# Kernel tuning notes

Measured on AMD Instinct MI355X. Metric: run time of the kernel, lower is better.

The kernel has to match this reference:

```python
import jax, jax.numpy as jnp
import numpy as np

B, Q, KV, D, H = 2, 2048, 2048, 1024, 16
DH = D // H  # 64


def _rmsnorm(x, w, eps):
    return x * jax.lax.rsqrt(jnp.mean(x * x, axis=-1, keepdims=True) + eps) * w


def setup_inputs() -> dict:
    k0 = jax.random.key(0)
    ks = jax.random.split(k0, 7)
    s = 0.02
    return {
        "query": jax.random.normal(ks[0], (B, Q, D), jnp.float32),
        "key": jax.random.normal(ks[1], (B, KV, D), jnp.float32),
        "value": jax.random.normal(ks[2], (B, KV, D), jnp.float32),
        # RMSNorm weights (init to ones like nn.RMSNorm)
        "wq_norm": jnp.ones((D,), jnp.float32),
        "wk_norm": jnp.ones((D,), jnp.float32),
        # MHA in-projection for q and k (Wv / out_proj never affect attn weights)
        "Wq": jax.random.normal(ks[3], (D, D), jnp.float32) * s,
        "Wk": jax.random.normal(ks[4], (D, D), jnp.float32) * s,
        "bq": jax.random.normal(ks[5], (D,), jnp.float32) * s,
        "bk": jax.random.normal(ks[6], (D,), jnp.float32) * s,
    }


def reference(query, key, value, wq_norm, wk_norm, Wq, Wk, bq, bk):
    eps = jnp.finfo(query.dtype).eps  # nn.RMSNorm default eps
    qn = _rmsnorm(query, wq_norm, eps)
    kn = _rmsnorm(key, wk_norm, eps)
    # MHA in-projections (torch Linear: x @ W.T + b), split into heads
    q = (qn @ Wq.T + bq).reshape(B, Q, H, DH)
    k = (kn @ Wk.T + bk).reshape(B, KV, H, DH)
    # per-head scaled dot-product scores [B,H,Q,KV]
    scores = jnp.einsum('bihd,bjhd->bhij', q, k) / np.float32(np.sqrt(DH))
    # softmax over keys, then average over heads (average_attn_weights=True)
    attn = jax.nn.softmax(scores, axis=-1).mean(axis=1)  # [B,Q,KV]
    # custom re-weighting of the *separate* value tensor
    features = jnp.einsum('bij,bjd->bid', attn, value)  # [B,Q,D]
    return features
```

## Files before the change

kernel.cpp:

```cpp
#include <hip/hip_runtime.h>

#define B_  2
#define Q_  2048
#define KV_ 2048
#define D_  1024
#define H_  16
#define DH_ 64

#define QSCALE 0.18033688011112042f

using u16 = unsigned short;
using bf16x8 = __attribute__((ext_vector_type(8))) short;
using f32x4  = __attribute__((ext_vector_type(4))) float;

__device__ __forceinline__ u16 f2bf(float x) {
  unsigned u = __float_as_uint(x);
  u += 0x7fffu + ((u >> 16) & 1u);
  return (u16)(u >> 16);
}

__device__ __forceinline__ void gl_lds16(const void* g, void* l) {
  __builtin_amdgcn_global_load_lds(
      (const __attribute__((address_space(1))) void*)g,
      (__attribute__((address_space(3))) void*)l, 16, 0, 0);
}

__device__ __forceinline__ int swz_off(int row, int unit) {
  return row * 64 + ((unit ^ (row & 7)) << 3);
}

#define MFMA16(a, b, c) __builtin_amdgcn_mfma_f32_16x16x32_bf16((a), (b), (c), 0, 0, 0)
#define EXP2F(x) __builtin_amdgcn_exp2f(x)

__global__ __launch_bounds__(256) void k_rmsnorm_cast(
    const float* __restrict__ q, const float* __restrict__ k,
    const float* __restrict__ wq, const float* __restrict__ wk,
    u16* __restrict__ qn, u16* __restrict__ kn)
{
  const int row = blockIdx.x;
  const float* src; const float* w; u16* dst;
  if (row < B_ * Q_) {
    src = q + (size_t)row * D_; w = wq; dst = qn + (size_t)row * D_;
  } else {
    const int r2 = row - B_ * Q_;
    src = k + (size_t)r2 * D_; w = wk; dst = kn + (size_t)r2 * D_;
  }
  const int t = threadIdx.x;
  float4 v = reinterpret_cast<const float4*>(src)[t];
  float ss = v.x * v.x + v.y * v.y + v.z * v.z + v.w * v.w;
  #pragma unroll
  for (int off = 1; off < 64; off <<= 1) ss += __shfl_xor(ss, off);
  __shared__ float red[4];
  if ((t & 63) == 0) red[t >> 6] = ss;
  __syncthreads();
  const float tot = red[0] + red[1] + red[2] + red[3];
  const float sc = rsqrtf(tot * (1.0f / D_) + 1.1920929e-07f);
  float4 wv = reinterpret_cast<const float4*>(w)[t];
  ushort4 o;
  o.x = f2bf(v.x * sc * wv.x);
  o.y = f2bf(v.y * sc * wv.y);
  o.z = f2bf(v.z * sc * wv.z);
  o.w = f2bf(v.w * sc * wv.w);
  reinterpret_cast<ushort4*>(dst)[t] = o;
}

__global__ __launch_bounds__(256) void k_prep_small(
    const float* __restrict__ Wq, const float* __restrict__ Wk,
    const float* __restrict__ bq, const float* __restrict__ bk,
    u16* __restrict__ Wb, float* __restrict__ biasbuf)
{
  const int bid = blockIdx.x, t = threadIdx.x;
  if (bid < 2048) {
    const int i = bid * 256 + t;
    const bool isK = i >= 262144;
    const int j = i & 262143;
    float4 v = reinterpret_cast<const float4*>(isK ? Wk : Wq)[j];
    ushort4 o;
    o.x = f2bf(v.x); o.y = f2bf(v.y); o.z = f2bf(v.z); o.w = f2bf(v.w);
    reinterpret_cast<ushort4*>(Wb + (isK ? D_ * D_ : 0))[j] = o;
  } else {
    #pragma unroll
    for (int r = 0; r < 2; ++r) {
      const int i = r * 256 + t;
      float4 v = (i < 256) ? reinterpret_cast<const float4*>(bq)[i]
                           : reinterpret_cast<const float4*>(bk)[i - 256];
      reinterpret_cast<float4*>(biasbuf)[i] = v;
    }
  }
}

__global__ __launch_bounds__(256) void k_transpose_cast_v(
    const float* __restrict__ v, u16* __restrict__ vT)
{
  const int kv0 = blockIdx.x * 64, d0 = blockIdx.y * 64, b = blockIdx.z;
  __shared__ u16 tile[64][72];
  const int t = threadIdx.x;
  #pragma unroll
  for (int i = 0; i < 16; ++i) {
    const int idx = i * 256 + t, r = idx >> 6, c = idx & 63;
    tile[r][c] = f2bf(v[((size_t)b * KV_ + kv0 + r) * D_ + d0 + c]);
  }
  __syncthreads();
  #pragma unroll
  for (int i = 0; i < 16; ++i) {
    const int idx = i * 256 + t, r = idx >> 6, c = idx & 63;
    vT[((size_t)b * D_ + d0 + r) * KV_ + kv0 + c] = tile[c][r];
  }
}

template<int TM, int TN, bool OUT_BF16, bool PROJ>
__global__ __launch_bounds__(256) void k_gemm_bt(
    const u16* __restrict__ A, int lda, long sA,
    const u16* __restrict__ Bm, int ldb, long sB,
    void* __restrict__ C, int ldc, long sC,
    int K, const float* __restrict__ bias)
{
  constexpr int MR = TM / 32, NR = TN / 32;
  const int bb = blockIdx.z;
  const u16* Ab = A + (size_t)bb * sA;
  const u16* Bb = Bm + (size_t)bb * sB;
  const int row0 = blockIdx.y * TM, col0 = blockIdx.x * TN;
  __shared__ u16 As[TM * 64];
  __shared__ u16 Bs[TN * 64];
  const int tid = threadIdx.x, lane = tid & 63;
  const int w = tid >> 6, wm = w >> 1, wn = w & 1;
  const int lrow = lane & 15, sub = lane >> 4, lrow7 = lrow & 7;
  const f32x4 zero4 = {0.f, 0.f, 0.f, 0.f};
  f32x4 acc[MR][NR];
  #pragma unroll
  for (int m = 0; m < MR; ++m)
    #pragma unroll
    for (int n = 0; n < NR; ++n) acc[m][n] = zero4;

  const int nk = K >> 6;
  for (int kt = 0; kt < nk; ++kt) {
    const int k0 = kt << 6;
    #pragma unroll
    for (int i = 0; i < TM / 32; ++i) {
      const int c = i * 256 + tid, r = c >> 3, u = (c & 7) ^ (r & 7);
      gl_lds16(Ab + (size_t)(row0 + r) * lda + k0 + u * 8, &As[c * 8]);
    }
    #pragma unroll
    for (int i = 0; i < TN / 32; ++i) {
      const int c = i * 256 + tid, r = c >> 3, u = (c & 7) ^ (r & 7);
      gl_lds16(Bb + (size_t)(col0 + r) * ldb + k0 + u * 8, &Bs[c * 8]);
    }
    __syncthreads();
    #pragma unroll
    for (int ks = 0; ks < 2; ++ks) {
      bf16x8 af[MR], bfr[NR];
      #pragma unroll
      for (int m = 0; m < MR; ++m) {
        const int rA = wm * (TM / 2) + m * 16 + lrow;
        af[m] = *(const bf16x8*)&As[rA * 64 + ((((ks << 2) + sub) ^ lrow7) << 3)];
      }
      #pragma unroll
      for (int n = 0; n < NR; ++n) {
        const int rB = wn * (TN / 2) + n * 16 + lrow;
        bfr[n] = *(const bf16x8*)&Bs[rB * 64 + ((((ks << 2) + sub) ^ lrow7) << 3)];
      }
      #pragma unroll
      for (int m = 0; m < MR; ++m)
        #pragma unroll
        for (int n = 0; n < NR; ++n)
          acc[m][n] = MFMA16(af[m], bfr[n], acc[m][n]);
    }
    __syncthreads();
  }
  const int crow = sub * 4, ccol = lane & 15;
  const float scl = (PROJ && bb == 0) ? QSCALE : 1.0f;
  #pragma unroll
  for (int m = 0; m < MR; ++m) {
    #pragma unroll
    for (int n = 0; n < NR; ++n) {
      const int gcol = col0 + wn * (TN / 2) + n * 16 + ccol;
      const float badd = PROJ ? bias[bb * 1024 + gcol] : 0.0f;
      #pragma unroll
      for (int r = 0; r < 4; ++r) {
        const int grow = row0 + wm * (TM / 2) + m * 16 + crow + r;
        const float val = (acc[m][n][r] + badd) * scl;
        if (OUT_BF16)
          ((u16*)C)[(size_t)bb * sC + (size_t)grow * ldc + gcol] = f2bf(val);
        else
          ((float*)C)[(size_t)bb * sC + (size_t)grow * ldc + gcol] = val;
      }
    }
  }
}

__global__ __launch_bounds__(256) void k_attn_rowsum(
    const u16* __restrict__ qp, const u16* __restrict__ kp,
    float* __restrict__ Linv)
{
  const int qb = blockIdx.x * 64, h = blockIdx.y, b = blockIdx.z;
  __shared__ u16 Ks[128 * 64];
  const int tid = threadIdx.x, lane = tid & 63, w = tid >> 6;
  const int lrow = lane & 15, sub = lane >> 4;
  const size_t qoff = ((size_t)b * Q_ + qb + w * 16 + lrow) * D_ + h * 64 + sub * 8;
  const bf16x8 af0 = *(const bf16x8*)&qp[qoff];
  const bf16x8 af1 = *(const bf16x8*)&qp[qoff + 32];
  const f32x4 zero4 = {0.f, 0.f, 0.f, 0.f};
  float lsum[4] = {0.f, 0.f, 0.f, 0.f};
  for (int kt = 0; kt < KV_ / 128; ++kt) {
    const int kv0 = kt * 128;
    #pragma unroll
    for (int i = 0; i < 4; ++i) {
      const int c = i * 256 + tid, r = c >> 3, u = (c & 7) ^ (r & 7);
      gl_lds16(&kp[((size_t)b * KV_ + kv0 + r) * D_ + h * 64 + u * 8], &Ks[c * 8]);
    }
    __syncthreads();
    #pragma unroll
    for (int c = 0; c < 8; ++c) {
      const bf16x8 b0 = *(const bf16x8*)&Ks[swz_off(c * 16 + lrow, sub)];
      const bf16x8 b1 = *(const bf16x8*)&Ks[swz_off(c * 16 + lrow, 4 + sub)];
      f32x4 s = zero4;
      s = MFMA16(af0, b0, s);
      s = MFMA16(af1, b1, s);
      #pragma unroll
      for (int r = 0; r < 4; ++r) lsum[r] += EXP2F(s[r]);
    }
    __syncthreads();
  }
  #pragma unroll
  for (int r = 0; r < 4; ++r) {
    #pragma unroll
    for (int off = 1; off < 16; off <<= 1) lsum[r] += __shfl_xor(lsum[r], off);
  }
  if ((lane & 15) == 0) {
    const int grow = qb + w * 16 + sub * 4;
    #pragma unroll
    for (int r = 0; r < 4; ++r)
      Linv[((size_t)b * H_ + h) * Q_ + grow + r] = 1.0f / (lsum[r] * (float)H_);
  }
}

__global__ __launch_bounds__(256) void k_attn_weights(
    const u16* __restrict__ qp, const u16* __restrict__ kp,
    const float* __restrict__ Linv, u16* __restrict__ attn)
{
  const int kv0 = blockIdx.x * 128, qb = blockIdx.y * 64, b = blockIdx.z;
  __shared__ u16 Ks[128 * 64];
  const int tid = threadIdx.x, lane = tid & 63, w = tid >> 6;
  const int lrow = lane & 15, sub = lane >> 4;
  const int growb = qb + w * 16 + sub * 4;
  const f32x4 zero4 = {0.f, 0.f, 0.f, 0.f};
  f32x4 acc[8];
  #pragma unroll
  for (int c = 0; c < 8; ++c) acc[c] = zero4;

  for (int h = 0; h < H_; ++h) {
    if (h) __syncthreads();
    #pragma unroll
    for (int i = 0; i < 4; ++i) {
      const int c = i * 256 + tid, r = c >> 3, u = (c & 7) ^ (r & 7);
      gl_lds16(&kp[((size_t)b * KV_ + kv0 + r) * D_ + h * 64 + u * 8], &Ks[c * 8]);
    }
    const size_t qoff = ((size_t)b * Q_ + qb + w * 16 + lrow) * D_ + h * 64 + sub * 8;
    const bf16x8 af0 = *(const bf16x8*)&qp[qoff];
    const bf16x8 af1 = *(const bf16x8*)&qp[qoff + 32];
    const float4 linv = *reinterpret_cast<const float4*>(
        &Linv[((size_t)b * H_ + h) * Q_ + growb]);
    __syncthreads();
    #pragma unroll
    for (int c = 0; c < 8; ++c) {
      const bf16x8 b0 = *(const bf16x8*)&Ks[swz_off(c * 16 + lrow, sub)];
      const bf16x8 b1 = *(const bf16x8*)&Ks[swz_off(c * 16 + lrow, 4 + sub)];
      f32x4 s = zero4;
      s = MFMA16(af0, b0, s);
      s = MFMA16(af1, b1, s);
      acc[c][0] += EXP2F(s[0]) * linv.x;
      acc[c][1] += EXP2F(s[1]) * linv.y;
      acc[c][2] += EXP2F(s[2]) * linv.z;
      acc[c][3] += EXP2F(s[3]) * linv.w;
    }
  }
  #pragma unroll
  for (int c = 0; c < 8; ++c) {
    const int gcol = kv0 + c * 16 + (lane & 15);
    #pragma unroll
    for (int r = 0; r < 4; ++r)
      attn[((size_t)b * Q_ + growb + r) * KV_ + gcol] = f2bf(acc[c][r]);
  }
}

extern "C" void kernel_launch(void* const* d_in, const int* in_sizes, int n_in,
                              void* d_out, int out_size, void* d_ws, size_t ws_size,
                              hipStream_t stream)
{
  (void)in_sizes; (void)n_in; (void)out_size; (void)ws_size;
  const float* query = (const float*)d_in[0];
  const float* key   = (const float*)d_in[1];
  const float* value = (const float*)d_in[2];
  const float* wqn   = (const float*)d_in[3];
  const float* wkn   = (const float*)d_in[4];
  const float* Wq    = (const float*)d_in[5];
  const float* Wk    = (const float*)d_in[6];
  const float* bq    = (const float*)d_in[7];
  const float* bk    = (const float*)d_in[8];
  float* out = (float*)d_out;

  char* ws = (char*)d_ws;
  u16* qn   = (u16*)(ws);
  u16* attn = (u16*)(ws);
  u16* qp   = (u16*)(ws + 16777216);
  u16* kp   = (u16*)(ws + 25165824);
  u16* Wqb  = (u16*)(ws + 33554432);
  u16* vT   = (u16*)(ws + 37748736);
  float* Linv = (float*)(ws + 46137344);
  float* biasbuf = (float*)(ws + 46399488);
  u16* kn = qn + 4194304;

  k_rmsnorm_cast<<<dim3(B_ * Q_ + B_ * KV_), dim3(256), 0, stream>>>(
      query, key, wqn, wkn, qn, kn);
  k_prep_small<<<dim3(2049), dim3(256), 0, stream>>>(Wq, Wk, bq, bk, Wqb, biasbuf);
  k_transpose_cast_v<<<dim3(KV_ / 64, D_ / 64, B_), dim3(256), 0, stream>>>(value, vT);

  k_gemm_bt<128, 128, true, true>
      <<<dim3(D_ / 128, (B_ * Q_) / 128, 2), dim3(256), 0, stream>>>(
      qn, D_, 4194304, Wqb, D_, 1048576, qp, D_, 4194304, D_, biasbuf);

  k_attn_rowsum<<<dim3(Q_ / 64, H_, B_), dim3(256), 0, stream>>>(qp, kp, Linv);
  k_attn_weights<<<dim3(KV_ / 128, Q_ / 64, B_), dim3(256), 0, stream>>>(qp, kp, Linv, attn);

  k_gemm_bt<128, 64, false, false>
      <<<dim3(D_ / 64, Q_ / 128, B_), dim3(256), 0, stream>>>(
      attn, KV_, (long)Q_ * KV_, vT, KV_, (long)D_ * KV_,
      out, D_, (long)Q_ * D_, KV_, nullptr);
}
```

Before: 147.5 us.

## Double-buffer LDS tiles and remap waves to split KV columns in attention kernels

Adds double-buffered shared-memory staging to the GEMM, rowsum and attention-weight kernels. The next K tile or head is loaded while the current one is computed, and one of the two barriers per iteration is removed. In the attention kernels, each wave now covers all 64 query rows over a 32-column KV slice instead of 16 rows over all 128 columns, which changes the Q and K fragment reuse. The rowsum kernel therefore needs a cross-wave LDS reduction. The change doubles LDS use and raises register pressure, which could lower occupancy.

New measurement: 207.4 us. 40.6% more time.

```diff
diff --git a/kernel.cpp b/kernel.cpp
--- a/kernel.cpp
+++ b/kernel.cpp
@@ -120,8 +120,8 @@
   const u16* Ab = A + (size_t)bb * sA;
   const u16* Bb = Bm + (size_t)bb * sB;
   const int row0 = blockIdx.y * TM, col0 = blockIdx.x * TN;
-  __shared__ u16 As[TM * 64];
-  __shared__ u16 Bs[TN * 64];
+  __shared__ u16 As[2][TM * 64];
+  __shared__ u16 Bs[2][TN * 64];
   const int tid = threadIdx.x, lane = tid & 63;
   const int w = tid >> 6, wm = w >> 1, wn = w & 1;
   const int lrow = lane & 15, sub = lane >> 4, lrow7 = lrow & 7;
@@ -133,31 +133,39 @@
     for (int n = 0; n < NR; ++n) acc[m][n] = zero4;
 
   const int nk = K >> 6;
+
+#define GEMM_STAGE(buf, kt)                                                   \
+  {                                                                           \
+    const int k0 = (kt) << 6;                                                 \
+    _Pragma("unroll")                                                         \
+    for (int i = 0; i < TM / 32; ++i) {                                       \
+      const int c = i * 256 + tid, r = c >> 3, u = (c & 7) ^ (r & 7);         \
+      gl_lds16(Ab + (size_t)(row0 + r) * lda + k0 + u * 8, &As[buf][c * 8]);  \
+    }                                                                         \
+    _Pragma("unroll")                                                         \
+    for (int i = 0; i < TN / 32; ++i) {                                       \
+      const int c = i * 256 + tid, r = c >> 3, u = (c & 7) ^ (r & 7);         \
+      gl_lds16(Bb + (size_t)(col0 + r) * ldb + k0 + u * 8, &Bs[buf][c * 8]);  \
+    }                                                                         \
+  }
+
+  GEMM_STAGE(0, 0);
+  int cur = 0;
   for (int kt = 0; kt < nk; ++kt) {
-    const int k0 = kt << 6;
-    #pragma unroll
-    for (int i = 0; i < TM / 32; ++i) {
-      const int c = i * 256 + tid, r = c >> 3, u = (c & 7) ^ (r & 7);
-      gl_lds16(Ab + (size_t)(row0 + r) * lda + k0 + u * 8, &As[c * 8]);
-    }
-    #pragma unroll
-    for (int i = 0; i < TN / 32; ++i) {
-      const int c = i * 256 + tid, r = c >> 3, u = (c & 7) ^ (r & 7);
-      gl_lds16(Bb + (size_t)(col0 + r) * ldb + k0 + u * 8, &Bs[c * 8]);
-    }
     __syncthreads();
+    if (kt + 1 < nk) GEMM_STAGE(cur ^ 1, kt + 1);
     #pragma unroll
     for (int ks = 0; ks < 2; ++ks) {
       bf16x8 af[MR], bfr[NR];
       #pragma unroll
       for (int m = 0; m < MR; ++m) {
         const int rA = wm * (TM / 2) + m * 16 + lrow;
-        af[m] = *(const bf16x8*)&As[rA * 64 + ((((ks << 2) + sub) ^ lrow7) << 3)];
+        af[m] = *(const bf16x8*)&As[cur][rA * 64 + ((((ks << 2) + sub) ^ lrow7) << 3)];
       }
       #pragma unroll
       for (int n = 0; n < NR; ++n) {
         const int rB = wn * (TN / 2) + n * 16 + lrow;
-        bfr[n] = *(const bf16x8*)&Bs[rB * 64 + ((((ks << 2) + sub) ^ lrow7) << 3)];
+        bfr[n] = *(const bf16x8*)&Bs[cur][rB * 64 + ((((ks << 2) + sub) ^ lrow7) << 3)];
       }
       #pragma unroll
       for (int m = 0; m < MR; ++m)
@@ -165,8 +173,10 @@
         for (int n = 0; n < NR; ++n)
           acc[m][n] = MFMA16(af[m], bfr[n], acc[m][n]);
     }
-    __syncthreads();
-  }
+    cur ^= 1;
+  }
+#undef GEMM_STAGE
+
   const int crow = sub * 4, ccol = lane & 15;
   const float scl = (PROJ && bb == 0) ? QSCALE : 1.0f;
   #pragma unroll
@@ -188,49 +198,79 @@
   }
 }
 
+#define STAGE_K(buf, kvbase, hh)                                              \
+  {                                                                           \
+    _Pragma("unroll")                                                         \
+    for (int i = 0; i < 4; ++i) {                                             \
+      const int c = i * 256 + tid, r = c >> 3, u = (c & 7) ^ (r & 7);         \
+      gl_lds16(&kp[((size_t)b * KV_ + (kvbase) + r) * D_ + (hh) * 64 + u * 8],\
+               &Ks[buf][c * 8]);                                              \
+    }                                                                         \
+  }
+
 __global__ __launch_bounds__(256) void k_attn_rowsum(
     const u16* __restrict__ qp, const u16* __restrict__ kp,
     float* __restrict__ Linv)
 {
   const int qb = blockIdx.x * 64, h = blockIdx.y, b = blockIdx.z;
-  __shared__ u16 Ks[128 * 64];
+  __shared__ u16 Ks[2][128 * 64];
+  __shared__ float red[4][64];
   const int tid = threadIdx.x, lane = tid & 63, w = tid >> 6;
   const int lrow = lane & 15, sub = lane >> 4;
-  const size_t qoff = ((size_t)b * Q_ + qb + w * 16 + lrow) * D_ + h * 64 + sub * 8;
-  const bf16x8 af0 = *(const bf16x8*)&qp[qoff];
-  const bf16x8 af1 = *(const bf16x8*)&qp[qoff + 32];
+
+  bf16x8 af[4][2];
+  #pragma unroll
+  for (int m = 0; m < 4; ++m)
+    #pragma unroll
+    for (int ks = 0; ks < 2; ++ks)
+      af[m][ks] = *(const bf16x8*)&qp[((size_t)b * Q_ + qb + m * 16 + lrow) * D_
+                                      + h * 64 + ks * 32 + sub * 8];
   const f32x4 zero4 = {0.f, 0.f, 0.f, 0.f};
-  float lsum[4] = {0.f, 0.f, 0.f, 0.f};
+  float lsum[4][4];
+  #pragma unroll
+  for (int m = 0; m < 4; ++m)
+    #pragma unroll
+    for (int r = 0; r < 4; ++r) lsum[m][r] = 0.f;
+
+  STAGE_K(0, 0, h);
+  int cur = 0;
   for (int kt = 0; kt < KV_ / 128; ++kt) {
-    const int kv0 = kt * 128;
-    #pragma unroll
-    for (int i = 0; i < 4; ++i) {
-      const int c = i * 256 + tid, r = c >> 3, u = (c & 7) ^ (r & 7);
-      gl_lds16(&kp[((size_t)b * KV_ + kv0 + r) * D_ + h * 64 + u * 8], &Ks[c * 8]);
-    }
     __syncthreads();
-    #pragma unroll
-    for (int c = 0; c < 8; ++c) {
-      const bf16x8 b0 = *(const bf16x8*)&Ks[swz_off(c * 16 + lrow, sub)];
-      const bf16x8 b1 = *(const bf16x8*)&Ks[swz_off(c * 16 + lrow, 4 + sub)];
-      f32x4 s = zero4;
-      s = MFMA16(af0, b0, s);
-      s = MFMA16(af1, b1, s);
-      #pragma unroll
-      for (int r = 0; r < 4; ++r) lsum[r] += EXP2F(s[r]);
-    }
-    __syncthreads();
-  }
-  #pragma unroll
-  for (int r = 0; r < 4; ++r) {
-    #pragma unroll
-    for (int off = 1; off < 16; off <<= 1) lsum[r] += __shfl_xor(lsum[r], off);
-  }
-  if ((lane & 15) == 0) {
-    const int grow = qb + w * 16 + sub * 4;
-    #pragma unroll
-    for (int r = 0; r < 4; ++r)
-      Linv[((size_t)b * H_ + h) * Q_ + grow + r] = 1.0f / (lsum[r] * (float)H_);
+    if (kt + 1 < KV_ / 128) STAGE_K(cur ^ 1, (kt + 1) * 128, h);
+    #pragma unroll
+    for (int n = 0; n < 2; ++n) {
+      const int row = w * 32 + n * 16 + lrow;
+      const bf16x8 b0 = *(const bf16x8*)&Ks[cur][swz_off(row, sub)];
+      const bf16x8 b1 = *(const bf16x8*)&Ks[cur][swz_off(row, 4 + sub)];
+      #pragma unroll
+      for (int m = 0; m < 4; ++m) {
+        f32x4 s = zero4;
+        s = MFMA16(af[m][0], b0, s);
+        s = MFMA16(af[m][1], b1, s);
+        #pragma unroll
+        for (int r = 0; r < 4; ++r) lsum[m][r] += EXP2F(s[r]);
+      }
+    }
+    cur ^= 1;
+  }
+  #pragma unroll
+  for (int m = 0; m < 4; ++m)
+    #pragma unroll
+    for (int r = 0; r < 4; ++r) {
+      #pragma unroll
+      for (int off = 1; off < 16; off <<= 1)
+        lsum[m][r] += __shfl_xor(lsum[m][r], off);
+    }
+  if (lrow == 0) {
+    #pragma unroll
+    for (int m = 0; m < 4; ++m)
+      #pragma unroll
+      for (int r = 0; r < 4; ++r) red[w][m * 16 + sub * 4 + r] = lsum[m][r];
+  }
+  __syncthreads();
+  if (tid < 64) {
+    const float s = red[0][tid] + red[1][tid] + red[2][tid] + red[3][tid];
+    Linv[((size_t)b * H_ + h) * Q_ + qb + tid] = 1.0f / (s * (float)H_);
   }
 }
 
@@ -239,47 +279,59 @@
     const float* __restrict__ Linv, u16* __restrict__ attn)
 {
   const int kv0 = blockIdx.x * 128, qb = blockIdx.y * 64, b = blockIdx.z;
-  __shared__ u16 Ks[128 * 64];
+  __shared__ u16 Ks[2][128 * 64];
   const int tid = threadIdx.x, lane = tid & 63, w = tid >> 6;
   const int lrow = lane & 15, sub = lane >> 4;
-  const int growb = qb + w * 16 + sub * 4;
   const f32x4 zero4 = {0.f, 0.f, 0.f, 0.f};
-  f32x4 acc[8];
-  #pragma unroll
-  for (int c = 0; c < 8; ++c) acc[c] = zero4;
-
+  f32x4 acc[4][2];
+  #pragma unroll
+  for (int m = 0; m < 4; ++m)
+    #pragma unroll
+    for (int n = 0; n < 2; ++n) acc[m][n] = zero4;
+
+  STAGE_K(0, kv0, 0);
+  int cur = 0;
   for (int h = 0; h < H_; ++h) {
-    if (h) __syncthreads();
-    #pragma unroll
-    for (int i = 0; i < 4; ++i) {
-      const int c = i * 256 + tid, r = c >> 3, u = (c & 7) ^ (r & 7);
-      gl_lds16(&kp[((size_t)b * KV_ + kv0 + r) * D_ + h * 64 + u * 8], &Ks[c * 8]);
-    }
-    const size_t qoff = ((size_t)b * Q_ + qb + w * 16 + lrow) * D_ + h * 64 + sub * 8;
-    const bf16x8 af0 = *(const bf16x8*)&qp[qoff];
-    const bf16x8 af1 = *(const bf16x8*)&qp[qoff + 32];
-    const float4 linv = *reinterpret_cast<const float4*>(
-        &Linv[((size_t)b * H_ + h) * Q_ + growb]);
     __syncthreads();
-    #pragma unroll
-    for (int c = 0; c < 8; ++c) {
-      const bf16x8 b0 = *(const bf16x8*)&Ks[swz_off(c * 16 + lrow, sub)];
-      const bf16x8 b1 = *(const bf16x8*)&Ks[swz_off(c * 16 + lrow, 4 + sub)];
-      f32x4 s = zero4;
-      s = MFMA16(af0, b0, s);
-      s = MFMA16(af1, b1, s);
-      acc[c][0] += EXP2F(s[0]) * linv.x;
-      acc[c][1] += EXP2F(s[1]) * linv.y;
-      acc[c][2] += EXP2F(s[2]) * linv.z;
-      acc[c][3] += EXP2F(s[3]) * linv.w;
-    }
-  }
-  #pragma unroll
-  for (int c = 0; c < 8; ++c) {
-    const int gcol = kv0 + c * 16 + (lane & 15);
-    #pragma unroll
-    for (int r = 0; r < 4; ++r)
-      attn[((size_t)b * Q_ + growb + r) * KV_ + gcol] = f2bf(acc[c][r]);
+    bf16x8 af[4][2];
+    #pragma unroll
+    for (int m = 0; m < 4; ++m)
+      #pragma unroll
+      for (int ks = 0; ks < 2; ++ks)
+        af[m][ks] = *(const bf16x8*)&qp[((size_t)b * Q_ + qb + m * 16 + lrow) * D_
+                                        + h * 64 + ks * 32 + sub * 8];
+    f32x4 lv[4];
+    #pragma unroll
+    for (int m = 0; m < 4; ++m)
+      lv[m] = *(const f32x4*)&Linv[((size_t)b * H_ + h) * Q_ + qb + m * 16 + sub * 4];
+    if (h + 1 < H_) STAGE_K(cur ^ 1, kv0, h + 1);
+    #pragma unroll
+    for (int n = 0; n < 2; ++n) {
+      const int row = w * 32 + n * 16 + lrow;
+      const bf16x8 b0 = *(const bf16x8*)&Ks[cur][swz_off(row, sub)];
+      const bf16x8 b1 = *(const bf16x8*)&Ks[cur][swz_off(row, 4 + sub)];
+      #pragma unroll
+      for (int m = 0; m < 4; ++m) {
+        f32x4 s = zero4;
+        s = MFMA16(af[m][0], b0, s);
+        s = MFMA16(af[m][1], b1, s);
+        #pragma unroll
+        for (int r = 0; r < 4; ++r) acc[m][n][r] += EXP2F(s[r]) * lv[m][r];
+      }
+    }
+    cur ^= 1;
+  }
+  #pragma unroll
+  for (int m = 0; m < 4; ++m) {
+    #pragma unroll
+    for (int n = 0; n < 2; ++n) {
+      const int gcol = kv0 + w * 32 + n * 16 + (lane & 15);
+      #pragma unroll
+      for (int r = 0; r < 4; ++r) {
+        const int grow = qb + m * 16 + sub * 4 + r;
+        attn[((size_t)b * Q_ + grow) * KV_ + gcol] = f2bf(acc[m][n][r]);
+      }
+    }
   }
 }
 
```
